# Optimization experiments

Measured on AMD Instinct MI355X. Metric: run time of the kernel, lower is better.

Reference implementation:

```python
import jax, jax.numpy as jnp
import numpy as np

B, S, DM, H = 8, 1024, 1024, 16
D = DM // H  # head dim = 64


def setup_inputs() -> dict:
    key = jax.random.key(0)
    ks = jax.random.split(key, 10)
    Q = jax.random.normal(ks[0], (B, S, DM), jnp.float32)
    K = jax.random.normal(ks[1], (B, S, DM), jnp.float32)
    V = jax.random.normal(ks[2], (B, S, DM), jnp.float32)
    pad = jax.random.randint(ks[3], (B,), 0, 512)
    sc = 0.02
    Wq = jax.random.normal(ks[4], (H, DM, D), jnp.float32) * sc
    Wk = jax.random.normal(ks[5], (H, DM, D), jnp.float32) * sc
    Wv = jax.random.normal(ks[6], (H, DM, D), jnp.float32) * sc
    bq = jnp.zeros((H, D), jnp.float32)
    bk = jnp.zeros((H, D), jnp.float32)
    bv = jnp.zeros((H, D), jnp.float32)
    Wo = jax.random.normal(ks[7], (DM, DM), jnp.float32) * sc
    bo = jnp.zeros((DM,), jnp.float32)
    return {"Q": Q, "K": K, "V": V, "pad": pad,
            "Wq": Wq, "bq": bq, "Wk": Wk, "bk": bk,
            "Wv": Wv, "bv": bv, "Wo": Wo, "bo": bo}


def reference(Q, K, V, pad, Wq, bq, Wk, bk, Wv, bv, Wo, bo):
    seq = Q.shape[1]
    # per-head projections, batched over heads: [B,H,S,D]
    Qh = jnp.einsum('bsm,hmd->bhsd', Q, Wq) + bq[None, :, None, :]
    Kh = jnp.einsum('bsm,hmd->bhsd', K, Wk) + bk[None, :, None, :]
    Vh = jnp.einsum('bsm,hmd->bhsd', V, Wv) + bv[None, :, None, :]
    # NOTE: original divides by sqrt(seq_len) (K.shape[1]), not sqrt(head_dim)
    scores = jnp.einsum('bhsd,bhtd->bhst', Qh, Kh) / jnp.sqrt(jnp.float32(seq))
    t = jnp.arange(seq)
    # padding mask over keys: last pad[b] positions; pad==0 masks ALL (torch -0: quirk)
    pad_mask = (t[None, :] >= seq - pad[:, None]) | (pad[:, None] == 0)  # [B,T]
    causal = t[None, :] > t[:, None]  # [S,T], strict upper triangle
    M = jnp.maximum(pad_mask[:, None, None, :].astype(jnp.float32),
                    causal[None, None, :, :].astype(jnp.float32))
    scores = scores + M * (-1e9)
    att = jax.nn.softmax(scores, axis=-1)
    Xh = jnp.einsum('bhst,bhtd->bhsd', att, Vh)
    # concat heads along last dim (head order preserved)
    X = Xh.transpose(0, 2, 1, 3).reshape(Q.shape[0], seq, H * D)
    return X @ Wo + bo
```

## Files before the change

### kernel.cpp

```cpp
#include <hip/hip_runtime.h>
#include <cmath>

#define BATCH 8
#define SEQ 1024
#define DMODEL 1024
#define NHEAD 16
#define HDIM 64

typedef _Float16 f16x8 __attribute__((ext_vector_type(8)));
typedef _Float16 f16x4 __attribute__((ext_vector_type(4)));
typedef _Float16 f16x2 __attribute__((ext_vector_type(2)));
typedef float    f32x4 __attribute__((ext_vector_type(4)));

template<int ALAYOUT, int BLAYOUT, int OLAYOUT>
__device__ __forceinline__
void gemm_body(const float* __restrict__ A, const float* __restrict__ Bm,
               const float* __restrict__ bias, float* __restrict__ C,
               int M, int N, int K)
{
    constexpr int BM = 128, BN = 128, BK = 64;
    alignas(16) __shared__ _Float16 As[128][72];
    alignas(16) __shared__ _Float16 Bs[128 * 72];

    const int t    = threadIdx.x;
    const int lane = t & 63;
    const int w    = t >> 6;
    const int wr   = w >> 1, wc = w & 1;
    const int q    = lane >> 4, r = lane & 15;
    const int m0   = blockIdx.y * BM;
    const int n0   = blockIdx.x * BN;

    f32x4 acc[4][4];
    #pragma unroll
    for (int i = 0; i < 4; ++i)
        #pragma unroll
        for (int j = 0; j < 4; ++j)
            acc[i][j] = (f32x4){0.f, 0.f, 0.f, 0.f};

    for (int kt = 0; kt < K / BK; ++kt) {
        const int k0 = kt * BK;
        __syncthreads();
        {
            const int kq = (t & 15) << 2;
            #pragma unroll
            for (int j = 0; j < 8; ++j) {
                const int row = (t >> 4) + j * 16;
                const float* src;
                if (ALAYOUT == 0) {
                    src = &A[(size_t)(m0 + row) * K + k0 + kq];
                } else {
                    const int gm = m0 + row;
                    const int bb = gm >> 10, s = gm & 1023;
                    const int h = (k0 + kq) >> 6, d = (k0 + kq) & 63;
                    src = &A[((((size_t)bb * NHEAD + h) << 10) + s) * HDIM + d];
                }
                const float4 v = *(const float4*)src;
                f16x4 hv = { (_Float16)v.x, (_Float16)v.y,
                             (_Float16)v.z, (_Float16)v.w };
                *(f16x4*)&As[row][kq] = hv;
            }
        }
        {
            const int n4 = (t & 31) << 2;
            const int kb = (t >> 5) << 3;
            #pragma unroll
            for (int j = 0; j < 2; ++j) {
                const int k4 = kb + j * 4;
                float4 v[4];
                #pragma unroll
                for (int rr = 0; rr < 4; ++rr) {
                    const float* src;
                    if (BLAYOUT == 0) {
                        const int n = n0 + n4;
                        const int h = n >> 6, d = n & 63;
                        src = &Bm[((size_t)h * K + (k0 + k4 + rr)) * HDIM + d];
                    } else {
                        src = &Bm[(size_t)(k0 + k4 + rr) * N + n0 + n4];
                    }
                    v[rr] = *(const float4*)src;
                }
                const int slot = k4 >> 3;
                #pragma unroll
                for (int c = 0; c < 4; ++c) {
                    const int n  = n4 + c;
                    const int sw = (n >> 1) & 7;
                    _Float16* dst = &Bs[0] + n * 72 + ((slot ^ sw) << 3) + (k4 & 7);
                    f16x4 hv = { (_Float16)(((const float*)&v[0])[c]),
                                 (_Float16)(((const float*)&v[1])[c]),
                                 (_Float16)(((const float*)&v[2])[c]),
                                 (_Float16)(((const float*)&v[3])[c]) };
                    *(f16x4*)dst = hv;
                }
            }
        }
        __syncthreads();
        #pragma unroll
        for (int h = 0; h < 2; ++h) {
            f16x8 a[4], b[4];
            #pragma unroll
            for (int mf = 0; mf < 4; ++mf) {
                const int mrow = wr * 64 + mf * 16 + r;
                a[mf] = *(const f16x8*)&As[mrow][h * 32 + q * 8];
            }
            #pragma unroll
            for (int nf = 0; nf < 4; ++nf) {
                const int n  = wc * 64 + nf * 16 + r;
                const int p  = (h * 4 + q) ^ ((n >> 1) & 7);
                b[nf] = *(const f16x8*)(&Bs[0] + n * 72 + (p << 3));
            }
            #pragma unroll
            for (int mf = 0; mf < 4; ++mf)
                #pragma unroll
                for (int nf = 0; nf < 4; ++nf)
                    acc[mf][nf] = __builtin_amdgcn_mfma_f32_16x16x32_f16(
                        a[mf], b[nf], acc[mf][nf], 0, 0, 0);
        }
    }

    #pragma unroll
    for (int mf = 0; mf < 4; ++mf) {
        #pragma unroll
        for (int nf = 0; nf < 4; ++nf) {
            const int col = n0 + wc * 64 + nf * 16 + r;
            const float bv = bias[col];
            #pragma unroll
            for (int i = 0; i < 4; ++i) {
                const int row = m0 + wr * 64 + mf * 16 + q * 4 + i;
                const float val = acc[mf][nf][i] + bv;
                if (OLAYOUT == 0) {
                    const int bb = row >> 10, s = row & 1023;
                    const int h = col >> 6, d = col & 63;
                    C[((((size_t)bb * NHEAD + h) << 10) + s) * HDIM + d] = val;
                } else {
                    C[(size_t)row * N + col] = val;
                }
            }
        }
    }
}

__global__ __launch_bounds__(256)
void gemm_qkv(const float* __restrict__ Q, const float* __restrict__ K,
              const float* __restrict__ V,
              const float* __restrict__ Wq, const float* __restrict__ Wk,
              const float* __restrict__ Wv,
              const float* __restrict__ bq, const float* __restrict__ bk,
              const float* __restrict__ bv,
              float* __restrict__ Qh, float* __restrict__ Kh,
              float* __restrict__ Vh, int M, int N, int Kd)
{
    const int z = blockIdx.z;
    const float* A    = (z == 0) ? Q  : (z == 1) ? K  : V;
    const float* B    = (z == 0) ? Wq : (z == 1) ? Wk : Wv;
    const float* bias = (z == 0) ? bq : (z == 1) ? bk : bv;
    float*       C    = (z == 0) ? Qh : (z == 1) ? Kh : Vh;
    gemm_body<0, 0, 0>(A, B, bias, C, M, N, Kd);
}

__global__ __launch_bounds__(256)
void gemm_out(const float* __restrict__ A, const float* __restrict__ Bm,
              const float* __restrict__ bias, float* __restrict__ C,
              int M, int N, int K)
{
    gemm_body<1, 1, 1>(A, Bm, bias, C, M, N, K);
}

__global__ __launch_bounds__(512, 4)
void attn_mfma(float* __restrict__ QX, const float* __restrict__ Kh,
               const float* __restrict__ Vh, const int* __restrict__ pad)
{
    alignas(16) __shared__ _Float16 Klds[64][72];
    alignas(16) __shared__ _Float16 VT[64][72];
    alignas(16) __shared__ _Float16 Plds[8][16][72];

    const int tid  = threadIdx.x;
    const int w    = tid >> 6;
    const int lane = tid & 63;
    const int qq   = lane >> 4;
    const int r    = lane & 15;
    const int bh   = blockIdx.y;
    const int b    = bh >> 4;
    const int s0   = blockIdx.x << 7;
    const int padb = pad[b];
    const size_t base = (size_t)bh * SEQ * HDIM;
    const int mrow = s0 + w * 16;

    f16x8 qf[2];
    #pragma unroll
    for (int kh = 0; kh < 2; ++kh) {
        const float* src = &QX[base + (size_t)(mrow + r) * HDIM + kh * 32 + qq * 8];
        const float4 v0 = *(const float4*)src;
        const float4 v1 = *(const float4*)(src + 4);
        qf[kh] = (f16x8){ (_Float16)v0.x, (_Float16)v0.y, (_Float16)v0.z, (_Float16)v0.w,
                          (_Float16)v1.x, (_Float16)v1.y, (_Float16)v1.z, (_Float16)v1.w };
    }

    const int kvlim = (padb == 0) ? SEQ : (SEQ - padb);
    const int Lblk  = (padb == 0) ? SEQ : min(s0 + 128, SEQ - padb);
    const int nt    = (Lblk + 63) >> 6;

    float mrun[4], lrun[4];
    f32x4 accO[4];
    #pragma unroll
    for (int i = 0; i < 4; ++i) {
        mrun[i] = -3.0e38f; lrun[i] = 0.f;
        accO[i] = (f32x4){0.f, 0.f, 0.f, 0.f};
    }

    for (int kt = 0; kt < nt; ++kt) {
        const int t0 = kt << 6;
        __syncthreads();
        {
            const int tk = tid >> 3, d8 = (tid & 7) << 3;
            const float* src = &Kh[base + (size_t)(t0 + tk) * HDIM + d8];
            const float4 v0 = *(const float4*)src;
            const float4 v1 = *(const float4*)(src + 4);
            *(f16x8*)&Klds[tk][d8] =
                (f16x8){ (_Float16)v0.x, (_Float16)v0.y, (_Float16)v0.z, (_Float16)v0.w,
                         (_Float16)v1.x, (_Float16)v1.y, (_Float16)v1.z, (_Float16)v1.w };
        }
        {
            const int tp = tid >> 4, dq = tid & 15;
            const float* src = &Vh[base + (size_t)(t0 + 2 * tp) * HDIM + 4 * dq];
            const float4 a0 = *(const float4*)src;
            const float4 a1 = *(const float4*)(src + HDIM);
            const float* f0 = (const float*)&a0;
            const float* f1 = (const float*)&a1;
            #pragma unroll
            for (int c = 0; c < 4; ++c)
                *(f16x2*)&VT[4 * dq + c][2 * tp] =
                    (f16x2){ (_Float16)f0[c], (_Float16)f1[c] };
        }
        __syncthreads();

        f32x4 sacc[4];
        #pragma unroll
        for (int tg = 0; tg < 4; ++tg) sacc[tg] = (f32x4){0.f, 0.f, 0.f, 0.f};
        #pragma unroll
        for (int tg = 0; tg < 4; ++tg)
            #pragma unroll
            for (int kh = 0; kh < 2; ++kh) {
                const f16x8 kf = *(const f16x8*)&Klds[tg * 16 + r][kh * 32 + qq * 8];
                sacc[tg] = __builtin_amdgcn_mfma_f32_16x16x32_f16(qf[kh], kf, sacc[tg], 0, 0, 0);
            }

        float sc[4][4];
        #pragma unroll
        for (int tg = 0; tg < 4; ++tg) {
            const int tt = t0 + tg * 16 + r;
            #pragma unroll
            for (int i = 0; i < 4; ++i) {
                const int mm = mrow + qq * 4 + i;
                float x = sacc[tg][i] * 0.03125f;
                if (tt > mm || tt >= kvlim || padb == 0)
                    x -= 1.0e9f;
                sc[tg][i] = x;
            }
        }
        float p[4][4], scale[4];
        #pragma unroll
        for (int i = 0; i < 4; ++i) {
            float mx = fmaxf(fmaxf(sc[0][i], sc[1][i]), fmaxf(sc[2][i], sc[3][i]));
            #pragma unroll
            for (int off = 1; off < 16; off <<= 1)
                mx = fmaxf(mx, __shfl_xor(mx, off));
            const float mn = fmaxf(mrun[i], mx);
            scale[i] = __expf(mrun[i] - mn);
            mrun[i] = mn;
            float ls = 0.f;
            #pragma unroll
            for (int tg = 0; tg < 4; ++tg) {
                const float pv = __expf(sc[tg][i] - mn);
                p[tg][i] = pv;
                ls += pv;
            }
            #pragma unroll
            for (int off = 1; off < 16; off <<= 1)
                ls += __shfl_xor(ls, off);
            lrun[i] = lrun[i] * scale[i] + ls;
        }

        #pragma unroll
        for (int tg = 0; tg < 4; ++tg)
            #pragma unroll
            for (int i = 0; i < 4; ++i)
                Plds[w][qq * 4 + i][tg * 16 + r] = (_Float16)p[tg][i];
        asm volatile("s_waitcnt lgkmcnt(0)" ::: "memory");
        __builtin_amdgcn_wave_barrier();

        const f16x8 pa0 = *(const f16x8*)&Plds[w][r][qq * 8];
        const f16x8 pa1 = *(const f16x8*)&Plds[w][r][32 + qq * 8];

        #pragma unroll
        for (int dg = 0; dg < 4; ++dg) {
            #pragma unroll
            for (int i = 0; i < 4; ++i) accO[dg][i] *= scale[i];
            const f16x8 v0f = *(const f16x8*)&VT[dg * 16 + r][qq * 8];
            const f16x8 v1f = *(const f16x8*)&VT[dg * 16 + r][32 + qq * 8];
            accO[dg] = __builtin_amdgcn_mfma_f32_16x16x32_f16(pa0, v0f, accO[dg], 0, 0, 0);
            accO[dg] = __builtin_amdgcn_mfma_f32_16x16x32_f16(pa1, v1f, accO[dg], 0, 0, 0);
        }
    }

    #pragma unroll
    for (int dg = 0; dg < 4; ++dg)
        #pragma unroll
        for (int i = 0; i < 4; ++i)
            QX[base + (size_t)(mrow + qq * 4 + i) * HDIM + dg * 16 + r] =
                accO[dg][i] / lrun[i];
}

extern "C" void kernel_launch(void* const* d_in, const int* in_sizes, int n_in,
                              void* d_out, int out_size, void* d_ws, size_t ws_size,
                              hipStream_t stream)
{
    const float* Q  = (const float*)d_in[0];
    const float* K  = (const float*)d_in[1];
    const float* V  = (const float*)d_in[2];
    const int*  pad = (const int*)d_in[3];
    const float* Wq = (const float*)d_in[4];
    const float* bq = (const float*)d_in[5];
    const float* Wk = (const float*)d_in[6];
    const float* bk = (const float*)d_in[7];
    const float* Wv = (const float*)d_in[8];
    const float* bv = (const float*)d_in[9];
    const float* Wo = (const float*)d_in[10];
    const float* bo = (const float*)d_in[11];
    float* out = (float*)d_out;

    float* ws = (float*)d_ws;
    const size_t per = (size_t)BATCH * NHEAD * SEQ * HDIM;
    float* Qh = ws;
    float* Kh = ws + per;
    float* Vh = ws + 2 * per;

    const int M = BATCH * SEQ;
    dim3 gq(DMODEL / 128, M / 128, 3);
    gemm_qkv<<<gq, 256, 0, stream>>>(Q, K, V, Wq, Wk, Wv, bq, bk, bv,
                                     Qh, Kh, Vh, M, DMODEL, DMODEL);

    attn_mfma<<<dim3(SEQ / 128, BATCH * NHEAD), 512, 0, stream>>>(Qh, Kh, Vh, pad);

    gemm_out<<<dim3(DMODEL / 128, M / 128), 256, 0, stream>>>(Qh, Wo, bo, out, M, DMODEL, DMODEL);
}
```

Baseline: 428.8 us.

## Pre-convert inputs to fp16, transpose weights, and load GEMM tiles directly into LDS

Two new prep kernels run first: one converts Q/K/V to fp16 and one writes transposed fp16 copies of all weight matrices. The GEMMs then stream fp16 tiles straight into LDS with global_load_lds, using an XOR swizzle applied on the global address side. Intermediates (Qh/Kh/Vh and the attention output X) are stored in fp16, and attention writes X directly in the concatenated [B,S,DM] layout, so the output GEMM needs no gather. This is meant to remove in-loop conversion work, strided weight access and fp32 intermediate traffic. In exchange it adds extra full passes over the inputs, reuses workspace buffers through aliasing, and keeps intermediates in fp16.

Measured after the change: 371.5 us. -13.4%, faster.

```diff
diff --git a/kernel.cpp b/kernel.cpp
--- a/kernel.cpp
+++ b/kernel.cpp
@@ -6,29 +6,83 @@
 #define DMODEL 1024
 #define NHEAD 16
 #define HDIM 64
+#define USE_GLOAD 1
 
 typedef _Float16 f16x8 __attribute__((ext_vector_type(8)));
 typedef _Float16 f16x4 __attribute__((ext_vector_type(4)));
 typedef _Float16 f16x2 __attribute__((ext_vector_type(2)));
 typedef float    f32x4 __attribute__((ext_vector_type(4)));
 
-template<int ALAYOUT, int BLAYOUT, int OLAYOUT>
-__device__ __forceinline__
-void gemm_body(const float* __restrict__ A, const float* __restrict__ Bm,
-               const float* __restrict__ bias, float* __restrict__ C,
-               int M, int N, int K)
-{
-    constexpr int BM = 128, BN = 128, BK = 64;
-    alignas(16) __shared__ _Float16 As[128][72];
-    alignas(16) __shared__ _Float16 Bs[128 * 72];
+
+__global__ __launch_bounds__(256)
+void prep_cvt(const float* __restrict__ Q, const float* __restrict__ K,
+              const float* __restrict__ V, _Float16* __restrict__ Qf,
+              _Float16* __restrict__ Kf, _Float16* __restrict__ Vf)
+{
+    const int n = (8192 * 1024) / 4;
+    const float*   src = (blockIdx.y == 0) ? Q : (blockIdx.y == 1) ? K : V;
+    _Float16*      dst = (blockIdx.y == 0) ? Qf : (blockIdx.y == 1) ? Kf : Vf;
+    for (int i = blockIdx.x * 256 + threadIdx.x; i < n; i += gridDim.x * 256) {
+        const float4 v = ((const float4*)src)[i];
+        ((f16x4*)dst)[i] = (f16x4){ (_Float16)v.x, (_Float16)v.y,
+                                    (_Float16)v.z, (_Float16)v.w };
+    }
+}
+
+__global__ __launch_bounds__(256)
+void prep_tr(const float* __restrict__ Wq, const float* __restrict__ Wk,
+             const float* __restrict__ Wv, const float* __restrict__ Wo,
+             _Float16* __restrict__ WqT, _Float16* __restrict__ WkT,
+             _Float16* __restrict__ WvT, _Float16* __restrict__ WoT)
+{
+    __shared__ float L[64][65];
+    const int z  = blockIdx.z;
+    const int t  = threadIdx.x;
+    const float*    W  = (z == 0) ? Wq : (z == 1) ? Wk : (z == 2) ? Wv : Wo;
+    _Float16*       WT = (z == 0) ? WqT : (z == 1) ? WkT : (z == 2) ? WvT : WoT;
+    const int k0 = blockIdx.y * 64;
+    const int n0 = blockIdx.x * 64;
+    const int kr = t >> 2, c4 = (t & 3) * 16;
+    const float* src = (z < 3)
+        ? &W[((size_t)blockIdx.x * DMODEL + (k0 + kr)) * HDIM + c4]
+        : &W[(size_t)(k0 + kr) * DMODEL + n0 + c4];
+    #pragma unroll
+    for (int j = 0; j < 4; ++j) {
+        const float4 v = *(const float4*)(src + j * 4);
+        L[kr][c4 + j * 4 + 0] = v.x; L[kr][c4 + j * 4 + 1] = v.y;
+        L[kr][c4 + j * 4 + 2] = v.z; L[kr][c4 + j * 4 + 3] = v.w;
+    }
+    __syncthreads();
+    const int d = t >> 2, kk = (t & 3) * 16;
+    f16x8 o0, o1;
+    #pragma unroll
+    for (int j = 0; j < 8; ++j) {
+        o0[j] = (_Float16)L[kk + j][d];
+        o1[j] = (_Float16)L[kk + 8 + j][d];
+    }
+    *(f16x8*)&WT[(size_t)(n0 + d) * DMODEL + k0 + kk]     = o0;
+    *(f16x8*)&WT[(size_t)(n0 + d) * DMODEL + k0 + kk + 8] = o1;
+}
+
+template<int OLAYOUT>
+__global__ __launch_bounds__(256)
+void gemm_f16(const _Float16* __restrict__ A, const _Float16* __restrict__ BT,
+              const float* __restrict__ bias, float* __restrict__ Cf,
+              _Float16* __restrict__ Ch)
+{
+    constexpr int Kd = DMODEL;
+    alignas(16) __shared__ _Float16 Al[128 * 64];
+    alignas(16) __shared__ _Float16 Bl[128 * 64];
 
     const int t    = threadIdx.x;
     const int lane = t & 63;
     const int w    = t >> 6;
     const int wr   = w >> 1, wc = w & 1;
     const int q    = lane >> 4, r = lane & 15;
-    const int m0   = blockIdx.y * BM;
-    const int n0   = blockIdx.x * BN;
+    const int m0   = blockIdx.y * 128;
+    const int n0   = blockIdx.x * 128;
+    const int srow = lane >> 3;
+    const int sslot = lane & 7;
 
     f32x4 acc[4][4];
     #pragma unroll
@@ -37,61 +91,37 @@
         for (int j = 0; j < 4; ++j)
             acc[i][j] = (f32x4){0.f, 0.f, 0.f, 0.f};
 
-    for (int kt = 0; kt < K / BK; ++kt) {
-        const int k0 = kt * BK;
-        __syncthreads();
-        {
-            const int kq = (t & 15) << 2;
-            #pragma unroll
-            for (int j = 0; j < 8; ++j) {
-                const int row = (t >> 4) + j * 16;
-                const float* src;
-                if (ALAYOUT == 0) {
-                    src = &A[(size_t)(m0 + row) * K + k0 + kq];
-                } else {
-                    const int gm = m0 + row;
-                    const int bb = gm >> 10, s = gm & 1023;
-                    const int h = (k0 + kq) >> 6, d = (k0 + kq) & 63;
-                    src = &A[((((size_t)bb * NHEAD + h) << 10) + s) * HDIM + d];
-                }
-                const float4 v = *(const float4*)src;
-                f16x4 hv = { (_Float16)v.x, (_Float16)v.y,
-                             (_Float16)v.z, (_Float16)v.w };
-                *(f16x4*)&As[row][kq] = hv;
-            }
-        }
-        {
-            const int n4 = (t & 31) << 2;
-            const int kb = (t >> 5) << 3;
-            #pragma unroll
-            for (int j = 0; j < 2; ++j) {
-                const int k4 = kb + j * 4;
-                float4 v[4];
-                #pragma unroll
-                for (int rr = 0; rr < 4; ++rr) {
-                    const float* src;
-                    if (BLAYOUT == 0) {
-                        const int n = n0 + n4;
-                        const int h = n >> 6, d = n & 63;
-                        src = &Bm[((size_t)h * K + (k0 + k4 + rr)) * HDIM + d];
-                    } else {
-                        src = &Bm[(size_t)(k0 + k4 + rr) * N + n0 + n4];
-                    }
-                    v[rr] = *(const float4*)src;
-                }
-                const int slot = k4 >> 3;
-                #pragma unroll
-                for (int c = 0; c < 4; ++c) {
-                    const int n  = n4 + c;
-                    const int sw = (n >> 1) & 7;
-                    _Float16* dst = &Bs[0] + n * 72 + ((slot ^ sw) << 3) + (k4 & 7);
-                    f16x4 hv = { (_Float16)(((const float*)&v[0])[c]),
-                                 (_Float16)(((const float*)&v[1])[c]),
-                                 (_Float16)(((const float*)&v[2])[c]),
-                                 (_Float16)(((const float*)&v[3])[c]) };
-                    *(f16x4*)dst = hv;
-                }
-            }
+    for (int kt = 0; kt < Kd / 64; ++kt) {
+        const int k0 = kt * 64;
+        #pragma unroll
+        for (int j = 0; j < 4; ++j) {
+            const int rowA = w * 32 + j * 8 + srow;
+            const int colA = ((sslot ^ (rowA & 7)) << 3);
+#if USE_GLOAD
+            __builtin_amdgcn_global_load_lds(
+                (const __attribute__((address_space(1))) void*)
+                    &A[(size_t)(m0 + rowA) * Kd + k0 + colA],
+                (__attribute__((address_space(3))) void*)&Al[(w * 32 + j * 8) * 64],
+                16, 0, 0);
+#else
+            *(f16x8*)&Al[(size_t)rowA * 64 + (sslot << 3)] =
+                *(const f16x8*)&A[(size_t)(m0 + rowA) * Kd + k0 + colA];
+#endif
+        }
+        #pragma unroll
+        for (int j = 0; j < 4; ++j) {
+            const int rowB = w * 32 + j * 8 + srow;
+            const int colB = ((sslot ^ (rowB & 7)) << 3);
+#if USE_GLOAD
+            __builtin_amdgcn_global_load_lds(
+                (const __attribute__((address_space(1))) void*)
+                    &BT[(size_t)(n0 + rowB) * Kd + k0 + colB],
+                (__attribute__((address_space(3))) void*)&Bl[(w * 32 + j * 8) * 64],
+                16, 0, 0);
+#else
+            *(f16x8*)&Bl[(size_t)rowB * 64 + (sslot << 3)] =
+                *(const f16x8*)&BT[(size_t)(n0 + rowB) * Kd + k0 + colB];
+#endif
         }
         __syncthreads();
         #pragma unroll
@@ -99,14 +129,13 @@
             f16x8 a[4], b[4];
             #pragma unroll
             for (int mf = 0; mf < 4; ++mf) {
-                const int mrow = wr * 64 + mf * 16 + r;
-                a[mf] = *(const f16x8*)&As[mrow][h * 32 + q * 8];
+                const int row = wr * 64 + mf * 16 + r;
+                a[mf] = *(const f16x8*)&Al[row * 64 + (((h * 4 + q) ^ (row & 7)) << 3)];
             }
             #pragma unroll
             for (int nf = 0; nf < 4; ++nf) {
-                const int n  = wc * 64 + nf * 16 + r;
-                const int p  = (h * 4 + q) ^ ((n >> 1) & 7);
-                b[nf] = *(const f16x8*)(&Bs[0] + n * 72 + (p << 3));
+                const int row = wc * 64 + nf * 16 + r;
+                b[nf] = *(const f16x8*)&Bl[row * 64 + (((h * 4 + q) ^ (row & 7)) << 3)];
             }
             #pragma unroll
             for (int mf = 0; mf < 4; ++mf)
@@ -115,6 +144,7 @@
                     acc[mf][nf] = __builtin_amdgcn_mfma_f32_16x16x32_f16(
                         a[mf], b[nf], acc[mf][nf], 0, 0, 0);
         }
+        __syncthreads();
     }
 
     #pragma unroll
@@ -130,46 +160,21 @@
                 if (OLAYOUT == 0) {
                     const int bb = row >> 10, s = row & 1023;
                     const int h = col >> 6, d = col & 63;
-                    C[((((size_t)bb * NHEAD + h) << 10) + s) * HDIM + d] = val;
+                    Ch[((((size_t)bb * NHEAD + h) << 10) + s) * HDIM + d] = (_Float16)val;
                 } else {
-                    C[(size_t)row * N + col] = val;
+                    Cf[(size_t)row * DMODEL + col] = val;
                 }
             }
         }
     }
 }
 
-__global__ __launch_bounds__(256)
-void gemm_qkv(const float* __restrict__ Q, const float* __restrict__ K,
-              const float* __restrict__ V,
-              const float* __restrict__ Wq, const float* __restrict__ Wk,
-              const float* __restrict__ Wv,
-              const float* __restrict__ bq, const float* __restrict__ bk,
-              const float* __restrict__ bv,
-              float* __restrict__ Qh, float* __restrict__ Kh,
-              float* __restrict__ Vh, int M, int N, int Kd)
-{
-    const int z = blockIdx.z;
-    const float* A    = (z == 0) ? Q  : (z == 1) ? K  : V;
-    const float* B    = (z == 0) ? Wq : (z == 1) ? Wk : Wv;
-    const float* bias = (z == 0) ? bq : (z == 1) ? bk : bv;
-    float*       C    = (z == 0) ? Qh : (z == 1) ? Kh : Vh;
-    gemm_body<0, 0, 0>(A, B, bias, C, M, N, Kd);
-}
-
-__global__ __launch_bounds__(256)
-void gemm_out(const float* __restrict__ A, const float* __restrict__ Bm,
-              const float* __restrict__ bias, float* __restrict__ C,
-              int M, int N, int K)
-{
-    gemm_body<1, 1, 1>(A, Bm, bias, C, M, N, K);
-}
-
 __global__ __launch_bounds__(512, 4)
-void attn_mfma(float* __restrict__ QX, const float* __restrict__ Kh,
-               const float* __restrict__ Vh, const int* __restrict__ pad)
-{
-    alignas(16) __shared__ _Float16 Klds[64][72];
+void attn_mfma(const _Float16* __restrict__ Qh, const _Float16* __restrict__ Kh,
+               const _Float16* __restrict__ Vh, const int* __restrict__ pad,
+               _Float16* __restrict__ X)
+{
+    alignas(16) __shared__ _Float16 Klds[64 * 64];
     alignas(16) __shared__ _Float16 VT[64][72];
     alignas(16) __shared__ _Float16 Plds[8][16][72];
 
@@ -180,6 +185,7 @@
     const int r    = lane & 15;
     const int bh   = blockIdx.y;
     const int b    = bh >> 4;
+    const int hh   = bh & 15;
     const int s0   = blockIdx.x << 7;
     const int padb = pad[b];
     const size_t base = (size_t)bh * SEQ * HDIM;
@@ -187,13 +193,8 @@
 
     f16x8 qf[2];
     #pragma unroll
-    for (int kh = 0; kh < 2; ++kh) {
-        const float* src = &QX[base + (size_t)(mrow + r) * HDIM + kh * 32 + qq * 8];
-        const float4 v0 = *(const float4*)src;
-        const float4 v1 = *(const float4*)(src + 4);
-        qf[kh] = (f16x8){ (_Float16)v0.x, (_Float16)v0.y, (_Float16)v0.z, (_Float16)v0.w,
-                          (_Float16)v1.x, (_Float16)v1.y, (_Float16)v1.z, (_Float16)v1.w };
-    }
+    for (int kh = 0; kh < 2; ++kh)
+        qf[kh] = *(const f16x8*)&Qh[base + (size_t)(mrow + r) * HDIM + kh * 32 + qq * 8];
 
     const int kvlim = (padb == 0) ? SEQ : (SEQ - padb);
     const int Lblk  = (padb == 0) ? SEQ : min(s0 + 128, SEQ - padb);
@@ -207,29 +208,29 @@
         accO[i] = (f32x4){0.f, 0.f, 0.f, 0.f};
     }
 
+    const int krow  = w * 8 + (lane >> 3);
+    const int kslot = lane & 7;
+    const int tp = tid >> 4, dq = tid & 15;
+
     for (int kt = 0; kt < nt; ++kt) {
         const int t0 = kt << 6;
         __syncthreads();
+#if USE_GLOAD
+        __builtin_amdgcn_global_load_lds(
+            (const __attribute__((address_space(1))) void*)
+                &Kh[base + (size_t)(t0 + krow) * HDIM + ((kslot ^ (krow & 7)) << 3)],
+            (__attribute__((address_space(3))) void*)&Klds[w * 8 * 64],
+            16, 0, 0);
+#else
+        *(f16x8*)&Klds[krow * 64 + (kslot << 3)] =
+            *(const f16x8*)&Kh[base + (size_t)(t0 + krow) * HDIM + ((kslot ^ (krow & 7)) << 3)];
+#endif
         {
-            const int tk = tid >> 3, d8 = (tid & 7) << 3;
-            const float* src = &Kh[base + (size_t)(t0 + tk) * HDIM + d8];
-            const float4 v0 = *(const float4*)src;
-            const float4 v1 = *(const float4*)(src + 4);
-            *(f16x8*)&Klds[tk][d8] =
-                (f16x8){ (_Float16)v0.x, (_Float16)v0.y, (_Float16)v0.z, (_Float16)v0.w,
-                         (_Float16)v1.x, (_Float16)v1.y, (_Float16)v1.z, (_Float16)v1.w };
-        }
-        {
-            const int tp = tid >> 4, dq = tid & 15;
-            const float* src = &Vh[base + (size_t)(t0 + 2 * tp) * HDIM + 4 * dq];
-            const float4 a0 = *(const float4*)src;
-            const float4 a1 = *(const float4*)(src + HDIM);
-            const float* f0 = (const float*)&a0;
-            const float* f1 = (const float*)&a1;
+            const f16x4 a0 = *(const f16x4*)&Vh[base + (size_t)(t0 + 2 * tp) * HDIM + 4 * dq];
+            const f16x4 a1 = *(const f16x4*)&Vh[base + (size_t)(t0 + 2 * tp + 1) * HDIM + 4 * dq];
             #pragma unroll
             for (int c = 0; c < 4; ++c)
-                *(f16x2*)&VT[4 * dq + c][2 * tp] =
-                    (f16x2){ (_Float16)f0[c], (_Float16)f1[c] };
+                *(f16x2*)&VT[4 * dq + c][2 * tp] = (f16x2){ a0[c], a1[c] };
         }
         __syncthreads();
 
@@ -240,7 +241,9 @@
         for (int tg = 0; tg < 4; ++tg)
             #pragma unroll
             for (int kh = 0; kh < 2; ++kh) {
-                const f16x8 kf = *(const f16x8*)&Klds[tg * 16 + r][kh * 32 + qq * 8];
+                const int kr = tg * 16 + r;
+                const f16x8 kf = *(const f16x8*)
+                    &Klds[kr * 64 + (((kh * 4 + qq) ^ (kr & 7)) << 3)];
                 sacc[tg] = __builtin_amdgcn_mfma_f32_16x16x32_f16(qf[kh], kf, sacc[tg], 0, 0, 0);
             }
 
@@ -306,8 +309,8 @@
     for (int dg = 0; dg < 4; ++dg)
         #pragma unroll
         for (int i = 0; i < 4; ++i)
-            QX[base + (size_t)(mrow + qq * 4 + i) * HDIM + dg * 16 + r] =
-                accO[dg][i] / lrun[i];
+            X[((size_t)b * SEQ + (mrow + qq * 4 + i)) * DMODEL + hh * HDIM + dg * 16 + r] =
+                (_Float16)(accO[dg][i] / lrun[i]);
 }
 
 extern "C" void kernel_launch(void* const* d_in, const int* in_sizes, int n_in,
@@ -328,18 +331,29 @@
     const float* bo = (const float*)d_in[11];
     float* out = (float*)d_out;
 
-    float* ws = (float*)d_ws;
-    const size_t per = (size_t)BATCH * NHEAD * SEQ * HDIM;
-    float* Qh = ws;
-    float* Kh = ws + per;
-    float* Vh = ws + 2 * per;
-
-    const int M = BATCH * SEQ;
-    dim3 gq(DMODEL / 128, M / 128, 3);
-    gemm_qkv<<<gq, 256, 0, stream>>>(Q, K, V, Wq, Wk, Wv, bq, bk, bv,
-                                     Qh, Kh, Vh, M, DMODEL, DMODEL);
-
-    attn_mfma<<<dim3(SEQ / 128, BATCH * NHEAD), 512, 0, stream>>>(Qh, Kh, Vh, pad);
-
-    gemm_out<<<dim3(DMODEL / 128, M / 128), 256, 0, stream>>>(Qh, Wo, bo, out, M, DMODEL, DMODEL);
-}
+    char* ws = (char*)d_ws;
+    const size_t MB = 1024 * 1024;
+    _Float16* Qf16 = (_Float16*)(ws + 0 * MB);
+    _Float16* Kf16 = (_Float16*)(ws + 16 * MB);
+    _Float16* Vf16 = (_Float16*)(ws + 32 * MB);
+    _Float16* WqT  = (_Float16*)(ws + 48 * MB);
+    _Float16* WkT  = (_Float16*)(ws + 50 * MB);
+    _Float16* WvT  = (_Float16*)(ws + 52 * MB);
+    _Float16* WoT  = (_Float16*)(ws + 54 * MB);
+    _Float16* Qh   = (_Float16*)(ws + 56 * MB);
+    _Float16* Kh   = (_Float16*)(ws + 72 * MB);
+    _Float16* Vh   = (_Float16*)(ws + 0 * MB);
+    _Float16* X    = (_Float16*)(ws + 16 * MB);
+
+    prep_cvt<<<dim3(1024, 3), 256, 0, stream>>>(Q, K, V, Qf16, Kf16, Vf16);
+    prep_tr <<<dim3(16, 16, 4), 256, 0, stream>>>(Wq, Wk, Wv, Wo, WqT, WkT, WvT, WoT);
+
+    dim3 gg(DMODEL / 128, (BATCH * SEQ) / 128);
+    gemm_f16<0><<<gg, 256, 0, stream>>>(Qf16, WqT, bq, nullptr, Qh);
+    gemm_f16<0><<<gg, 256, 0, stream>>>(Kf16, WkT, bk, nullptr, Kh);
+    gemm_f16<0><<<gg, 256, 0, stream>>>(Vf16, WvT, bv, nullptr, Vh);
+
+    attn_mfma<<<dim3(SEQ / 128, BATCH * NHEAD), 512, 0, stream>>>(Qh, Kh, Vh, pad, X);
+
+    gemm_f16<1><<<gg, 256, 0, stream>>>(X, WoT, bo, out, nullptr);
+}
```
